# Optimization experiments

Measured on AMD Instinct MI355X. Metric: run time of the kernel, lower is better.

Reference implementation:

```python
import jax, jax.numpy as jnp
import numpy as np

T, H, F, E, K = 1024, 1024, 2048, 8, 2  # tokens, hidden, ffn_inter, experts, top_k


def setup_inputs() -> dict:
    key = jax.random.key(0)
    ks = jax.random.split(key, 7)
    return {
        "hidden_states": jax.random.normal(ks[0], (T, H), dtype=jnp.float32),
        "token_selected_experts": jax.random.randint(ks[1], (T, K), 0, E, dtype=jnp.int32),
        "token_final_scales": jax.random.uniform(ks[2], (T, K), dtype=jnp.float32),
        "w1": jax.random.normal(ks[3], (E, 2 * F, H), dtype=jnp.float32) * 0.02,  # gated fc1: [gate; linear]
        "b1": jax.random.normal(ks[4], (E, 2 * F), dtype=jnp.float32) * 0.02,
        "w2": jax.random.normal(ks[5], (E, H, F), dtype=jnp.float32) * 0.02,
        "b2": jax.random.normal(ks[6], (E, H), dtype=jnp.float32) * 0.02,
    }


def reference(hidden_states, token_selected_experts, token_final_scales, w1, b1, w2, b2):
    # Grouped GEMM fc1 over all experts: [T, E, 2F]
    h1 = jnp.einsum('th,efh->tef', hidden_states, w1) + b1[None]
    ffn = w2.shape[2]
    gate, lin = h1[..., :ffn], h1[..., ffn:]
    act = jax.nn.silu(gate) * lin                      # swiglu gated activation, [T, E, F]
    y_all = jnp.einsum('tef,ehf->teh', act, w2) + b2[None]  # fc2, [T, E, H]
    # Gather the top-k selected experts per token and combine with final scales
    sel = token_selected_experts.astype(jnp.int32)     # [T, K]
    y_sel = jnp.take_along_axis(y_all, sel[:, :, None], axis=1)  # [T, K, H]
    out = jnp.sum(y_sel * token_final_scales[:, :, None], axis=1)  # [T, H]
    return out
```

## Files before the change

kernel.cpp:

```cpp
#include <hip/hip_runtime.h>
#include <hip/hip_bf16.h>
#include <cstdint>
#include <cstddef>

#define TDIM 1024
#define HDIM 1024
#define FDIM 2048
#define NEXP 8
#define NENT 2048

typedef __bf16 bf16_t;
typedef __bf16 bf16x4 __attribute__((ext_vector_type(4)));
typedef __bf16 bf16x8 __attribute__((ext_vector_type(8)));
typedef float  f32x4  __attribute__((ext_vector_type(4)));

#define H_ELEMS  ((size_t)TDIM*HDIM)
#define W1_ELEMS ((size_t)NEXP*2*FDIM*HDIM)
#define W2_ELEMS ((size_t)NEXP*HDIM*FDIM)

#define WB_OFFSETS 0
#define WB_ETOK    64
#define WB_ESCALE  (WB_ETOK + NENT*4)
#define WB_ACT     16512
#define WB_H       (WB_ACT + (size_t)NENT*FDIM*2)
#define WB_W2BF    (WB_H + H_ELEMS*2)
#define WB_W1BF    (WB_W2BF + W2_ELEMS*2)
#define WB_NEED    (WB_W1BF + W1_ELEMS*2)

__device__ __forceinline__ void gload16(const void* g, void* l) {
  __builtin_amdgcn_global_load_lds((const __attribute__((address_space(1))) void*)g,
                                   (__attribute__((address_space(3))) void*)l, 16, 0, 0);
}

__device__ __forceinline__ bf16x8 cvt8(const float4 a, const float4 b) {
  bf16x8 o;
  o[0]=(bf16_t)a.x; o[1]=(bf16_t)a.y; o[2]=(bf16_t)a.z; o[3]=(bf16_t)a.w;
  o[4]=(bf16_t)b.x; o[5]=(bf16_t)b.y; o[6]=(bf16_t)b.z; o[7]=(bf16_t)b.w;
  return o;
}

__device__ __forceinline__ int segswz(int seg, int row) {
  return seg ^ (row & 3) ^ ((row >> 2) & 3);
}

__global__ void route_all(const int* __restrict__ sel, const float* __restrict__ scal,
                          int* __restrict__ offsets, int* __restrict__ etok,
                          float* __restrict__ escale) {
  __shared__ int cnt[NEXP], cnt2[NEXP], offs[NEXP+1];
  const int t = threadIdx.x;
  if (t < NEXP) { cnt[t] = 0; cnt2[t] = 0; }
  __syncthreads();
  int e8[8];
  #pragma unroll
  for (int q = 0; q < 8; q++) {
    int i = t*8 + q;
    e8[q] = sel[i];
    atomicAdd(&cnt[e8[q]], 1);
  }
  __syncthreads();
  if (t == 0) {
    int s = 0;
    for (int e = 0; e < NEXP; e++) { offs[e] = s; offsets[e] = s; s += cnt[e]; }
    offs[NEXP] = s; offsets[NEXP] = s;
  }
  __syncthreads();
  #pragma unroll
  for (int q = 0; q < 8; q++) {
    int i = t*8 + q;
    int e = e8[q];
    int pos = offs[e] + atomicAdd(&cnt2[e], 1);
    etok[pos]   = i >> 1;
    escale[pos] = scal[i];
  }
}

__global__ void convert_h(const float* __restrict__ h, bf16_t* __restrict__ hbf) {
  size_t idx = ((size_t)blockIdx.x*256 + threadIdx.x) * 8;
  float4 v0 = ((const float4*)(h + idx))[0];
  float4 v1 = ((const float4*)(h + idx))[1];
  *(bf16x8*)(hbf + idx) = cvt8(v0, v1);
}


__global__ __launch_bounds__(256, 3) void gemm1_v10(
    const bf16_t* __restrict__ hbf, const bf16_t* __restrict__ w1bf,
    const float* __restrict__ b1, const int* __restrict__ offsets,
    const int* __restrict__ etok, bf16_t* __restrict__ act)
{
  const int e   = blockIdx.y;
  const int off = offsets[e];
  const int nt  = offsets[e+1] - off;
  const int m0  = blockIdx.z * 128;
  if (m0 >= nt) return;
  const int n0  = blockIdx.x * 64;

  __shared__ __align__(16) bf16_t As[2][128*32];
  __shared__ __align__(16) bf16_t Bg[2][64*32];
  __shared__ __align__(16) bf16_t Bl[2][64*32];

  const int tid  = threadIdx.x;
  const int w    = tid >> 6, lane = tid & 63;
  const int quad = lane >> 4, lr = lane & 15;
  const int wm   = w >> 1,  wn = w & 1;

  const bf16_t* asrc0; const bf16_t* asrc1;
  int arow0, arow1;
  {
    const int r0 = 0*64 + w*16 + (lane >> 2);
    const int r1 = 1*64 + w*16 + (lane >> 2);
    const int s0 = segswz(lane & 3, r0);
    const int s1 = segswz(lane & 3, r1);
    int e0 = m0 + r0; if (e0 > nt-1) e0 = nt-1;
    int e1 = m0 + r1; if (e1 > nt-1) e1 = nt-1;
    asrc0 = hbf + (size_t)etok[off + e0]*HDIM + s0*8;
    asrc1 = hbf + (size_t)etok[off + e1]*HDIM + s1*8;
    arow0 = (0*64 + w*16)*32;
    arow1 = (1*64 + w*16)*32;
  }

  const bf16_t* gsrc; const bf16_t* lsrc;
  int bdst;
  {
    const int brow = w*16 + (lane >> 2);
    const int bseg = segswz(lane & 3, brow);
    gsrc = w1bf + ((size_t)e*2*FDIM + (size_t)(n0 + brow))*HDIM + bseg*8;
    lsrc = gsrc + (size_t)FDIM*HDIM;
    bdst = (w*16)*32;
  }

  int aoff[4], boff[2];
  #pragma unroll
  for (int i = 0; i < 4; i++) {
    const int r = wm*64 + i*16 + lr;
    aoff[i] = r*32 + (segswz(quad, r) << 3);
  }
  #pragma unroll
  for (int j = 0; j < 2; j++) {
    const int r = wn*32 + j*16 + lr;
    boff[j] = r*32 + (segswz(quad, r) << 3);
  }

  f32x4 accg[4][2] = {}, accl[4][2] = {};

#define G1_STAGE(K0, NXT)                                                     \
  { gload16(asrc0 + (K0), &As[NXT][arow0]);                                   \
    gload16(asrc1 + (K0), &As[NXT][arow1]);                                   \
    gload16(gsrc  + (K0), &Bg[NXT][bdst]);                                    \
    gload16(lsrc  + (K0), &Bl[NXT][bdst]); }

#define G1_MFMA(CUR)                                                          \
  { bf16x8 af[4], gf[2], lf[2];                                               \
    _Pragma("unroll")                                                         \
    for (int i = 0; i < 4; i++) af[i] = *(const bf16x8*)&As[CUR][aoff[i]];    \
    _Pragma("unroll")                                                         \
    for (int j = 0; j < 2; j++) {                                             \
      gf[j] = *(const bf16x8*)&Bg[CUR][boff[j]];                              \
      lf[j] = *(const bf16x8*)&Bl[CUR][boff[j]];                              \
    }                                                                         \
    _Pragma("unroll")                                                         \
    for (int i = 0; i < 4; i++)                                               \
      _Pragma("unroll")                                                       \
      for (int j = 0; j < 2; j++) {                                           \
        accg[i][j] = __builtin_amdgcn_mfma_f32_16x16x32_bf16(af[i], gf[j], accg[i][j], 0, 0, 0); \
        accl[i][j] = __builtin_amdgcn_mfma_f32_16x16x32_bf16(af[i], lf[j], accl[i][j], 0, 0, 0); \
      } }

#define G1_STEP(CUR)                                                          \
  { G1_STAGE(k0 + 32, (CUR)^1);                                               \
    __builtin_amdgcn_sched_barrier(0);                                        \
    G1_MFMA(CUR);                                                             \
    asm volatile("s_waitcnt vmcnt(0)" ::: "memory");                          \
    __builtin_amdgcn_sched_barrier(0);                                        \
    __builtin_amdgcn_s_barrier();                                             \
    __builtin_amdgcn_sched_barrier(0);                                        \
    k0 += 32; }

  G1_STAGE(0, 0);
  asm volatile("s_waitcnt vmcnt(0)" ::: "memory");
  __builtin_amdgcn_sched_barrier(0);
  __builtin_amdgcn_s_barrier();
  __builtin_amdgcn_sched_barrier(0);

  int k0 = 0;
  while (k0 < 960) {
    G1_STEP(0);
    G1_STEP(1);
  }
  G1_STEP(0);
  G1_MFMA(1);

#undef G1_STEP
#undef G1_MFMA
#undef G1_STAGE

  #pragma unroll
  for (int j = 0; j < 2; j++) {
    const int f = n0 + wn*32 + j*16 + lr;
    const float bg_ = b1[e*2*FDIM + f];
    const float bl_ = b1[e*2*FDIM + FDIM + f];
    #pragma unroll
    for (int i = 0; i < 4; i++) {
      #pragma unroll
      for (int r = 0; r < 4; r++) {
        const int m = wm*64 + i*16 + quad*4 + r;
        if (m0 + m < nt) {
          const float g = accg[i][j][r] + bg_;
          const float l = accl[i][j][r] + bl_;
          const float s = g / (1.f + __expf(-g)) * l;
          act[(size_t)(off + m0 + m)*FDIM + f] = (bf16_t)s;
        }
      }
    }
  }
}

__global__ __launch_bounds__(256, 3) void gemm2_v10(
    const bf16_t* __restrict__ act, const bf16_t* __restrict__ w2bf,
    const float* __restrict__ b2, const int* __restrict__ offsets,
    const int* __restrict__ etok, const float* __restrict__ escale,
    float* __restrict__ out)
{
  const int e   = blockIdx.y;
  const int off = offsets[e];
  const int nt  = offsets[e+1] - off;
  const int m0  = blockIdx.z * 128;
  if (m0 >= nt) return;
  const int n0  = (blockIdx.x >> 2) * 128;
  const int kc  = blockIdx.x & 3;
  const int kbeg = kc * (FDIM/4);

  __shared__ __align__(16) bf16_t As[2][128*32];
  __shared__ __align__(16) bf16_t Bs[2][128*32];

  const int tid  = threadIdx.x;
  const int w    = tid >> 6, lane = tid & 63;
  const int quad = lane >> 4, lr = lane & 15;
  const int wm   = w >> 1,  wn = w & 1;

  const bf16_t* asrc0; const bf16_t* asrc1;
  int arow0, arow1;
  {
    const int r0 = 0*64 + w*16 + (lane >> 2);
    const int r1 = 1*64 + w*16 + (lane >> 2);
    const int s0 = segswz(lane & 3, r0);
    const int s1 = segswz(lane & 3, r1);
    int e0 = m0 + r0; if (e0 > nt-1) e0 = nt-1;
    int e1 = m0 + r1; if (e1 > nt-1) e1 = nt-1;
    asrc0 = act + (size_t)(off + e0)*FDIM + kbeg + s0*8;
    asrc1 = act + (size_t)(off + e1)*FDIM + kbeg + s1*8;
    arow0 = (0*64 + w*16)*32;
    arow1 = (1*64 + w*16)*32;
  }

  const bf16_t* bsrc0; const bf16_t* bsrc1;
  int bdst0, bdst1;
  {
    const int r0 = w*32 + (lane >> 2);
    const int r1 = w*32 + 16 + (lane >> 2);
    const int s0 = segswz(lane & 3, r0);
    const int s1 = segswz(lane & 3, r1);
    bsrc0 = w2bf + ((size_t)e*HDIM + (size_t)(n0 + r0))*FDIM + kbeg + s0*8;
    bsrc1 = w2bf + ((size_t)e*HDIM + (size_t)(n0 + r1))*FDIM + kbeg + s1*8;
    bdst0 = (w*32)*32;
    bdst1 = (w*32 + 16)*32;
  }

  int aoff[4], boff[4];
  #pragma unroll
  for (int i = 0; i < 4; i++) {
    const int r = wm*64 + i*16 + lr;
    aoff[i] = r*32 + (segswz(quad, r) << 3);
  }
  #pragma unroll
  for (int j = 0; j < 4; j++) {
    const int r = wn*64 + j*16 + lr;
    boff[j] = r*32 + (segswz(quad, r) << 3);
  }

  f32x4 acc[4][4] = {};

#define G2_STAGE(K0, NXT)                                                     \
  { gload16(asrc0 + (K0), &As[NXT][arow0]);                                   \
    gload16(asrc1 + (K0), &As[NXT][arow1]);                                   \
    gload16(bsrc0 + (K0), &Bs[NXT][bdst0]);                                   \
    gload16(bsrc1 + (K0), &Bs[NXT][bdst1]); }

#define G2_MFMA(CUR)                                                          \
  { bf16x8 af[4], bfr[4];                                                     \
    _Pragma("unroll")                                                         \
    for (int i = 0; i < 4; i++) af[i] = *(const bf16x8*)&As[CUR][aoff[i]];    \
    _Pragma("unroll")                                                         \
    for (int j = 0; j < 4; j++) bfr[j] = *(const bf16x8*)&Bs[CUR][boff[j]];   \
    _Pragma("unroll")                                                         \
    for (int i = 0; i < 4; i++)                                               \
      _Pragma("unroll")                                                       \
      for (int j = 0; j < 4; j++)                                             \
        acc[i][j] = __builtin_amdgcn_mfma_f32_16x16x32_bf16(af[i], bfr[j], acc[i][j], 0, 0, 0); }

#define G2_STEP(CUR)                                                          \
  { G2_STAGE(k0 + 32, (CUR)^1);                                               \
    __builtin_amdgcn_sched_barrier(0);                                        \
    G2_MFMA(CUR);                                                             \
    asm volatile("s_waitcnt vmcnt(0)" ::: "memory");                          \
    __builtin_amdgcn_sched_barrier(0);                                        \
    __builtin_amdgcn_s_barrier();                                             \
    __builtin_amdgcn_sched_barrier(0);                                        \
    k0 += 32; }

  G2_STAGE(0, 0);
  asm volatile("s_waitcnt vmcnt(0)" ::: "memory");
  __builtin_amdgcn_sched_barrier(0);
  __builtin_amdgcn_s_barrier();
  __builtin_amdgcn_sched_barrier(0);

  int k0 = 0;
  while (k0 < 448) {
    G2_STEP(0);
    G2_STEP(1);
  }
  G2_STEP(0);
  G2_MFMA(1);

#undef G2_STEP
#undef G2_MFMA
#undef G2_STAGE

  #pragma unroll
  for (int i = 0; i < 4; i++) {
    #pragma unroll
    for (int r = 0; r < 4; r++) {
      const int m = wm*64 + i*16 + quad*4 + r;
      if (m0 + m < nt) {
        const int slot = off + m0 + m;
        const int t    = etok[slot];
        const float s  = escale[slot];
        #pragma unroll
        for (int j = 0; j < 4; j++) {
          const int n = n0 + wn*64 + j*16 + lr;
          float v = acc[i][j][r];
          if (kc == 0) v += b2[e*HDIM + n];
          atomicAdd(&out[(size_t)t*HDIM + n], s * v);
        }
      }
    }
  }
}

__global__ __launch_bounds__(256, 3) void gemm1_v8(
    const bf16_t* __restrict__ hbf, const float* __restrict__ w1,
    const float* __restrict__ b1, const int* __restrict__ offsets,
    const int* __restrict__ etok, bf16_t* __restrict__ act)
{
  const int e   = blockIdx.y;
  const int off = offsets[e];
  const int nt  = offsets[e+1] - off;
  const int m0  = blockIdx.z * 128;
  if (m0 >= nt) return;
  const int n0  = blockIdx.x * 64;

  __shared__ __align__(16) bf16_t As[2][128*32];
  __shared__ __align__(16) bf16_t Bg[2][64*32];
  __shared__ __align__(16) bf16_t Bl[2][64*32];

  const int tid  = threadIdx.x;
  const int w    = tid >> 6, lane = tid & 63;
  const int quad = lane >> 4, lr = lane & 15;
  const int wm   = w >> 1,  wn = w & 1;

  const bf16_t* asrc0; const bf16_t* asrc1;
  int arow0, arow1;
  {
    const int r0 = 0*64 + w*16 + (lane >> 2);
    const int r1 = 1*64 + w*16 + (lane >> 2);
    const int s0 = segswz(lane & 3, r0);
    const int s1 = segswz(lane & 3, r1);
    int e0 = m0 + r0; if (e0 > nt-1) e0 = nt-1;
    int e1 = m0 + r1; if (e1 > nt-1) e1 = nt-1;
    asrc0 = hbf + (size_t)etok[off + e0]*HDIM + s0*8;
    asrc1 = hbf + (size_t)etok[off + e1]*HDIM + s1*8;
    arow0 = (0*64 + w*16)*32;
    arow1 = (1*64 + w*16)*32;
  }

  const int br = tid >> 2, bs = tid & 3;
  const float* gsrc = w1 + ((size_t)e*2*FDIM + (size_t)(n0 + br))*HDIM + bs*8;
  const float* lsrc = gsrc + (size_t)FDIM*HDIM;
  const int bofs = br*32 + (segswz(bs, br) << 3);

  int aoff[4], boff[2];
  #pragma unroll
  for (int i = 0; i < 4; i++) {
    const int r = wm*64 + i*16 + lr;
    aoff[i] = r*32 + (segswz(quad, r) << 3);
  }
  #pragma unroll
  for (int j = 0; j < 2; j++) {
    const int r = wn*32 + j*16 + lr;
    boff[j] = r*32 + (segswz(quad, r) << 3);
  }

  f32x4 accg[4][2] = {}, accl[4][2] = {};
  float4 g4[2][2], l4[2][2];

#define F1_LOADB(SET, K0)                                                     \
  { const float4* p_ = (const float4*)(gsrc + (K0));                          \
    g4[SET][0]=p_[0]; g4[SET][1]=p_[1];                                       \
    const float4* q_ = (const float4*)(lsrc + (K0));                          \
    l4[SET][0]=q_[0]; l4[SET][1]=q_[1]; }
#define F1_WRITEB(NXT, SET)                                                   \
  { *(bf16x8*)&Bg[NXT][bofs] = cvt8(g4[SET][0], g4[SET][1]);                  \
    *(bf16x8*)&Bl[NXT][bofs] = cvt8(l4[SET][0], l4[SET][1]); }
#define F1_MFMA(CUR)                                                          \
  { bf16x8 af[4], gf[2], lf[2];                                               \
    _Pragma("unroll")                                                         \
    for (int i = 0; i < 4; i++) af[i] = *(const bf16x8*)&As[CUR][aoff[i]];    \
    _Pragma("unroll")                                                         \
    for (int j = 0; j < 2; j++) {                                             \
      gf[j] = *(const bf16x8*)&Bg[CUR][boff[j]];                              \
      lf[j] = *(const bf16x8*)&Bl[CUR][boff[j]];                              \
    }                                                                         \
    _Pragma("unroll")                                                         \
    for (int i = 0; i < 4; i++)                                               \
      _Pragma("unroll")                                                       \
      for (int j = 0; j < 2; j++) {                                           \
        accg[i][j] = __builtin_amdgcn_mfma_f32_16x16x32_bf16(af[i], gf[j], accg[i][j], 0, 0, 0); \
        accl[i][j] = __builtin_amdgcn_mfma_f32_16x16x32_bf16(af[i], lf[j], accl[i][j], 0, 0, 0); \
      } }

  F1_LOADB(0, 0);
  __builtin_amdgcn_sched_barrier(0);
  gload16(asrc0 + 0, &As[0][arow0]);
  gload16(asrc1 + 0, &As[0][arow1]);
  __builtin_amdgcn_sched_barrier(0);
  F1_WRITEB(0, 0);
  F1_LOADB(0, 32);
  F1_LOADB(1, 64);
  asm volatile("s_waitcnt vmcnt(8) lgkmcnt(0)" ::: "memory");
  __builtin_amdgcn_sched_barrier(0);
  __builtin_amdgcn_s_barrier();
  __builtin_amdgcn_sched_barrier(0);

#define F1_STEP(CUR, SET)                                                     \
  { F1_WRITEB((CUR)^1, SET);                                                  \
    __builtin_amdgcn_sched_barrier(0);                                        \
    gload16(asrc0 + k0 + 32, &As[(CUR)^1][arow0]);                            \
    gload16(asrc1 + k0 + 32, &As[(CUR)^1][arow1]);                            \
    __builtin_amdgcn_sched_barrier(0);                                        \
    F1_LOADB(SET, k0 + 96);                                                   \
    __builtin_amdgcn_sched_barrier(0);                                        \
    F1_MFMA(CUR);                                                             \
    asm volatile("s_waitcnt vmcnt(4) lgkmcnt(0)" ::: "memory");               \
    __builtin_amdgcn_sched_barrier(0);                                        \
    __builtin_amdgcn_s_barrier();                                             \
    __builtin_amdgcn_sched_barrier(0);                                        \
    k0 += 32; }

  int k0 = 0;
  while (k0 < 896) { F1_STEP(0, 0); F1_STEP(1, 1); }
  F1_STEP(0, 0);
  F1_WRITEB(0, 1);
  __builtin_amdgcn_sched_barrier(0);
  gload16(asrc0 + 960, &As[0][arow0]);
  gload16(asrc1 + 960, &As[0][arow1]);
  __builtin_amdgcn_sched_barrier(0);
  F1_MFMA(1);
  asm volatile("s_waitcnt vmcnt(0) lgkmcnt(0)" ::: "memory");
  __builtin_amdgcn_sched_barrier(0);
  __builtin_amdgcn_s_barrier();
  __builtin_amdgcn_sched_barrier(0);
  F1_WRITEB(1, 0);
  __builtin_amdgcn_sched_barrier(0);
  gload16(asrc0 + 992, &As[1][arow0]);
  gload16(asrc1 + 992, &As[1][arow1]);
  __builtin_amdgcn_sched_barrier(0);
  F1_MFMA(0);
  asm volatile("s_waitcnt vmcnt(0) lgkmcnt(0)" ::: "memory");
  __builtin_amdgcn_sched_barrier(0);
  __builtin_amdgcn_s_barrier();
  __builtin_amdgcn_sched_barrier(0);
  F1_MFMA(1);

#undef F1_STEP
#undef F1_MFMA
#undef F1_WRITEB
#undef F1_LOADB

  #pragma unroll
  for (int j = 0; j < 2; j++) {
    const int f = n0 + wn*32 + j*16 + lr;
    const float bg_ = b1[e*2*FDIM + f];
    const float bl_ = b1[e*2*FDIM + FDIM + f];
    #pragma unroll
    for (int i = 0; i < 4; i++) {
      #pragma unroll
      for (int r = 0; r < 4; r++) {
        const int m = wm*64 + i*16 + quad*4 + r;
        if (m0 + m < nt) {
          const float g = accg[i][j][r] + bg_;
          const float l = accl[i][j][r] + bl_;
          const float s = g / (1.f + __expf(-g)) * l;
          act[(size_t)(off + m0 + m)*FDIM + f] = (bf16_t)s;
        }
      }
    }
  }
}

__global__ __launch_bounds__(256, 3) void gemm2_v8(
    const bf16_t* __restrict__ act, const float* __restrict__ w2,
    const float* __restrict__ b2, const int* __restrict__ offsets,
    const int* __restrict__ etok, const float* __restrict__ escale,
    float* __restrict__ out)
{
  const int e   = blockIdx.y;
  const int off = offsets[e];
  const int nt  = offsets[e+1] - off;
  const int m0  = blockIdx.z * 128;
  if (m0 >= nt) return;
  const int n0  = (blockIdx.x >> 2) * 128;
  const int kc  = blockIdx.x & 3;
  const int kbeg = kc * (FDIM/4);

  __shared__ __align__(16) bf16_t As[2][128*32];
  __shared__ __align__(16) bf16_t Bs[2][128*32];

  const int tid  = threadIdx.x;
  const int w    = tid >> 6, lane = tid & 63;
  const int quad = lane >> 4, lr = lane & 15;
  const int wm   = w >> 1,  wn = w & 1;

  const bf16_t* asrc0; const bf16_t* asrc1;
  int arow0, arow1;
  {
    const int r0 = 0*64 + w*16 + (lane >> 2);
    const int r1 = 1*64 + w*16 + (lane >> 2);
    const int s0 = segswz(lane & 3, r0);
    const int s1 = segswz(lane & 3, r1);
    int e0 = m0 + r0; if (e0 > nt-1) e0 = nt-1;
    int e1 = m0 + r1; if (e1 > nt-1) e1 = nt-1;
    asrc0 = act + (size_t)(off + e0)*FDIM + kbeg + s0*8;
    asrc1 = act + (size_t)(off + e1)*FDIM + kbeg + s1*8;
    arow0 = (0*64 + w*16)*32;
    arow1 = (1*64 + w*16)*32;
  }

  const int br = tid >> 1, bc = tid & 1;
  const float* bsrc = w2 + ((size_t)e*HDIM + (size_t)(n0 + br))*FDIM + kbeg + bc*16;
  const int bofs0 = br*32 + (segswz(2*bc,   br) << 3);
  const int bofs1 = br*32 + (segswz(2*bc+1, br) << 3);

  int aoff[4], boff[4];
  #pragma unroll
  for (int i = 0; i < 4; i++) {
    const int r = wm*64 + i*16 + lr;
    aoff[i] = r*32 + (segswz(quad, r) << 3);
  }
  #pragma unroll
  for (int j = 0; j < 4; j++) {
    const int r = wn*64 + j*16 + lr;
    boff[j] = r*32 + (segswz(quad, r) << 3);
  }

  f32x4 acc[4][4] = {};
  float4 b4[2][4];

#define F2_LOADB(SET, K0)                                                     \
  { const float4* p_ = (const float4*)(bsrc + (K0));                          \
    b4[SET][0]=p_[0]; b4[SET][1]=p_[1]; b4[SET][2]=p_[2]; b4[SET][3]=p_[3]; }
#define F2_WRITEB(NXT, SET)                                                   \
  { *(bf16x8*)&Bs[NXT][bofs0] = cvt8(b4[SET][0], b4[SET][1]);                 \
    *(bf16x8*)&Bs[NXT][bofs1] = cvt8(b4[SET][2], b4[SET][3]); }
#define F2_MFMA(CUR)                                                          \
  { bf16x8 af[4], bfr[4];                                                     \
    _Pragma("unroll")                                                         \
    for (int i = 0; i < 4; i++) af[i] = *(const bf16x8*)&As[CUR][aoff[i]];    \
    _Pragma("unroll")                                                         \
    for (int j = 0; j < 4; j++) bfr[j] = *(const bf16x8*)&Bs[CUR][boff[j]];   \
    _Pragma("unroll")                                                         \
    for (int i = 0; i < 4; i++)                                               \
      _Pragma("unroll")                                                       \
      for (int j = 0; j < 4; j++)                                             \
        acc[i][j] = __builtin_amdgcn_mfma_f32_16x16x32_bf16(af[i], bfr[j], acc[i][j], 0, 0, 0); }

  F2_LOADB(0, 0);
  __builtin_amdgcn_sched_barrier(0);
  gload16(asrc0 + 0, &As[0][arow0]);
  gload16(asrc1 + 0, &As[0][arow1]);
  __builtin_amdgcn_sched_barrier(0);
  F2_WRITEB(0, 0);
  F2_LOADB(0, 32);
  F2_LOADB(1, 64);
  asm volatile("s_waitcnt vmcnt(8) lgkmcnt(0)" ::: "memory");
  __builtin_amdgcn_sched_barrier(0);
  __builtin_amdgcn_s_barrier();
  __builtin_amdgcn_sched_barrier(0);

#define F2_STEP(CUR, SET)                                                     \
  { F2_WRITEB((CUR)^1, SET);                                                  \
    __builtin_amdgcn_sched_barrier(0);                                        \
    gload16(asrc0 + k0 + 32, &As[(CUR)^1][arow0]);                            \
    gload16(asrc1 + k0 + 32, &As[(CUR)^1][arow1]);                            \
    __builtin_amdgcn_sched_barrier(0);                                        \
    F2_LOADB(SET, k0 + 96);                                                   \
    __builtin_amdgcn_sched_barrier(0);                                        \
    F2_MFMA(CUR);                                                             \
    asm volatile("s_waitcnt vmcnt(4) lgkmcnt(0)" ::: "memory");               \
    __builtin_amdgcn_sched_barrier(0);                                        \
    __builtin_amdgcn_s_barrier();                                             \
    __builtin_amdgcn_sched_barrier(0);                                        \
    k0 += 32; }

  int k0 = 0;
  while (k0 < 384) { F2_STEP(0, 0); F2_STEP(1, 1); }
  F2_STEP(0, 0);
  F2_WRITEB(0, 1);
  __builtin_amdgcn_sched_barrier(0);
  gload16(asrc0 + 448, &As[0][arow0]);
  gload16(asrc1 + 448, &As[0][arow1]);
  __builtin_amdgcn_sched_barrier(0);
  F2_MFMA(1);
  asm volatile("s_waitcnt vmcnt(0) lgkmcnt(0)" ::: "memory");
  __builtin_amdgcn_sched_barrier(0);
  __builtin_amdgcn_s_barrier();
  __builtin_amdgcn_sched_barrier(0);
  F2_WRITEB(1, 0);
  __builtin_amdgcn_sched_barrier(0);
  gload16(asrc0 + 480, &As[1][arow0]);
  gload16(asrc1 + 480, &As[1][arow1]);
  __builtin_amdgcn_sched_barrier(0);
  F2_MFMA(0);
  asm volatile("s_waitcnt vmcnt(0) lgkmcnt(0)" ::: "memory");
  __builtin_amdgcn_sched_barrier(0);
  __builtin_amdgcn_s_barrier();
  __builtin_amdgcn_sched_barrier(0);
  F2_MFMA(1);

#undef F2_STEP
#undef F2_MFMA
#undef F2_WRITEB
#undef F2_LOADB

  #pragma unroll
  for (int i = 0; i < 4; i++) {
    #pragma unroll
    for (int r = 0; r < 4; r++) {
      const int m = wm*64 + i*16 + quad*4 + r;
      if (m0 + m < nt) {
        const int slot = off + m0 + m;
        const int t    = etok[slot];
        const float s  = escale[slot];
        #pragma unroll
        for (int j = 0; j < 4; j++) {
          const int n = n0 + wn*64 + j*16 + lr;
          float v = acc[i][j][r];
          if (kc == 0) v += b2[e*HDIM + n];
          atomicAdd(&out[(size_t)t*HDIM + n], s * v);
        }
      }
    }
  }
}

extern "C" void kernel_launch(void* const* d_in, const int* in_sizes, int n_in,
                              void* d_out, int out_size, void* d_ws, size_t ws_size,
                              hipStream_t stream) {
  const float* hidden = (const float*)d_in[0];
  const int*   sel    = (const int*)d_in[1];
  const float* scal   = (const float*)d_in[2];
  const float* w1     = (const float*)d_in[3];
  const float* b1     = (const float*)d_in[4];
  const float* w2     = (const float*)d_in[5];
  const float* b2     = (const float*)d_in[6];
  float* out = (float*)d_out;

  char* ws = (char*)d_ws;
  int*    offsets = (int*)(ws + WB_OFFSETS);
  int*    etok    = (int*)(ws + WB_ETOK);
  float*  escale  = (float*)(ws + WB_ESCALE);
  bf16_t* act     = (bf16_t*)(ws + WB_ACT);
  bf16_t* hbf     = (bf16_t*)(ws + WB_H);
  bf16_t* w2bf    = (bf16_t*)(ws + WB_W2BF);
  bf16_t* w1bf    = (bf16_t*)(ws + WB_W1BF);

  hipMemsetAsync(d_out, 0, (size_t)out_size * sizeof(float), stream);

  route_all<<<1, 256, 0, stream>>>(sel, scal, offsets, etok, escale);
  convert_h<<<(int)(H_ELEMS/8/256), 256, 0, stream>>>(hidden, hbf);

  if (ws_size >= WB_NEED) {
    convert_h<<<(int)(W2_ELEMS/8/256), 256, 0, stream>>>(w2, w2bf);
    convert_h<<<(int)(W1_ELEMS/8/256), 256, 0, stream>>>(w1, w1bf);
    gemm1_v10<<<dim3(FDIM/64, NEXP, NENT/128), 256, 0, stream>>>(hbf, w1bf, b1, offsets, etok, act);
    gemm2_v10<<<dim3((HDIM/128)*4, NEXP, NENT/128), 256, 0, stream>>>(act, w2bf, b2, offsets, etok, escale, out);
  } else {
    gemm1_v8<<<dim3(FDIM/64, NEXP, NENT/128), 256, 0, stream>>>(hbf, w1, b1, offsets, etok, act);
    gemm2_v8<<<dim3((HDIM/128)*4, NEXP, NENT/128), 256, 0, stream>>>(act, w2, b2, offsets, etok, escale, out);
  }
}
```

Measured before the change: 358.3 us.

## Triple-buffer LDS staging in both expert GEMMs with prefetch distance two

Both grouped GEMM kernels move from double to triple shared-memory buffers and issue global-to-LDS loads two K-steps ahead. The per-step wait relaxes from vmcnt(0) to vmcnt(4), so one stage's loads can stay in flight while the MFMAs run. The goal is to hide more global-load latency behind compute. The cost is more LDS per block, which could limit occupancy at 3 blocks per CU, plus more complex prologue and epilogue scheduling.

```diff
diff --git a/kernel.cpp b/kernel.cpp
--- a/kernel.cpp
+++ b/kernel.cpp
@@ -82,7 +82,7 @@
 }
 
 
-__global__ __launch_bounds__(256, 3) void gemm1_v10(
+__global__ __launch_bounds__(256, 3) void gemm1_v11(
     const bf16_t* __restrict__ hbf, const bf16_t* __restrict__ w1bf,
     const float* __restrict__ b1, const int* __restrict__ offsets,
     const int* __restrict__ etok, bf16_t* __restrict__ act)
@@ -94,9 +94,9 @@
   if (m0 >= nt) return;
   const int n0  = blockIdx.x * 64;
 
-  __shared__ __align__(16) bf16_t As[2][128*32];
-  __shared__ __align__(16) bf16_t Bg[2][64*32];
-  __shared__ __align__(16) bf16_t Bl[2][64*32];
+  __shared__ __align__(16) bf16_t As[3][128*32];
+  __shared__ __align__(16) bf16_t Bg[3][64*32];
+  __shared__ __align__(16) bf16_t Bl[3][64*32];
 
   const int tid  = threadIdx.x;
   const int w    = tid >> 6, lane = tid & 63;
@@ -165,28 +165,34 @@
         accl[i][j] = __builtin_amdgcn_mfma_f32_16x16x32_bf16(af[i], lf[j], accl[i][j], 0, 0, 0); \
       } }
 
-#define G1_STEP(CUR)                                                          \
-  { G1_STAGE(k0 + 32, (CUR)^1);                                               \
+#define G1_STEP(CUR, NXT)                                                     \
+  { G1_STAGE(k0 + 64, NXT);                                                   \
     __builtin_amdgcn_sched_barrier(0);                                        \
     G1_MFMA(CUR);                                                             \
-    asm volatile("s_waitcnt vmcnt(0)" ::: "memory");                          \
+    asm volatile("s_waitcnt vmcnt(4)" ::: "memory");                          \
     __builtin_amdgcn_sched_barrier(0);                                        \
     __builtin_amdgcn_s_barrier();                                             \
     __builtin_amdgcn_sched_barrier(0);                                        \
     k0 += 32; }
 
   G1_STAGE(0, 0);
-  asm volatile("s_waitcnt vmcnt(0)" ::: "memory");
+  G1_STAGE(32, 1);
+  asm volatile("s_waitcnt vmcnt(4)" ::: "memory");
   __builtin_amdgcn_sched_barrier(0);
   __builtin_amdgcn_s_barrier();
   __builtin_amdgcn_sched_barrier(0);
 
   int k0 = 0;
   while (k0 < 960) {
-    G1_STEP(0);
-    G1_STEP(1);
-  }
-  G1_STEP(0);
+    G1_STEP(0, 2);
+    G1_STEP(1, 0);
+    G1_STEP(2, 1);
+  }
+  G1_MFMA(0);
+  asm volatile("s_waitcnt vmcnt(0)" ::: "memory");
+  __builtin_amdgcn_sched_barrier(0);
+  __builtin_amdgcn_s_barrier();
+  __builtin_amdgcn_sched_barrier(0);
   G1_MFMA(1);
 
 #undef G1_STEP
@@ -214,7 +220,7 @@
   }
 }
 
-__global__ __launch_bounds__(256, 3) void gemm2_v10(
+__global__ __launch_bounds__(256, 3) void gemm2_v11(
     const bf16_t* __restrict__ act, const bf16_t* __restrict__ w2bf,
     const float* __restrict__ b2, const int* __restrict__ offsets,
     const int* __restrict__ etok, const float* __restrict__ escale,
@@ -229,8 +235,8 @@
   const int kc  = blockIdx.x & 3;
   const int kbeg = kc * (FDIM/4);
 
-  __shared__ __align__(16) bf16_t As[2][128*32];
-  __shared__ __align__(16) bf16_t Bs[2][128*32];
+  __shared__ __align__(16) bf16_t As[3][128*32];
+  __shared__ __align__(16) bf16_t Bs[3][128*32];
 
   const int tid  = threadIdx.x;
   const int w    = tid >> 6, lane = tid & 63;
@@ -297,29 +303,37 @@
       for (int j = 0; j < 4; j++)                                             \
         acc[i][j] = __builtin_amdgcn_mfma_f32_16x16x32_bf16(af[i], bfr[j], acc[i][j], 0, 0, 0); }
 
-#define G2_STEP(CUR)                                                          \
-  { G2_STAGE(k0 + 32, (CUR)^1);                                               \
+#define G2_STEP(CUR, NXT)                                                     \
+  { G2_STAGE(k0 + 64, NXT);                                                   \
     __builtin_amdgcn_sched_barrier(0);                                        \
     G2_MFMA(CUR);                                                             \
-    asm volatile("s_waitcnt vmcnt(0)" ::: "memory");                          \
+    asm volatile("s_waitcnt vmcnt(4)" ::: "memory");                          \
     __builtin_amdgcn_sched_barrier(0);                                        \
     __builtin_amdgcn_s_barrier();                                             \
     __builtin_amdgcn_sched_barrier(0);                                        \
     k0 += 32; }
 
   G2_STAGE(0, 0);
+  G2_STAGE(32, 1);
+  asm volatile("s_waitcnt vmcnt(4)" ::: "memory");
+  __builtin_amdgcn_sched_barrier(0);
+  __builtin_amdgcn_s_barrier();
+  __builtin_amdgcn_sched_barrier(0);
+
+  int k0 = 0;
+  while (k0 < 384) {
+    G2_STEP(0, 2);
+    G2_STEP(1, 0);
+    G2_STEP(2, 1);
+  }
+  G2_STEP(0, 2);
+  G2_STEP(1, 0);
+  G2_MFMA(2);
   asm volatile("s_waitcnt vmcnt(0)" ::: "memory");
   __builtin_amdgcn_sched_barrier(0);
   __builtin_amdgcn_s_barrier();
   __builtin_amdgcn_sched_barrier(0);
-
-  int k0 = 0;
-  while (k0 < 448) {
-    G2_STEP(0);
-    G2_STEP(1);
-  }
-  G2_STEP(0);
-  G2_MFMA(1);
+  G2_MFMA(0);
 
 #undef G2_STEP
 #undef G2_MFMA
@@ -690,8 +704,8 @@
   if (ws_size >= WB_NEED) {
     convert_h<<<(int)(W2_ELEMS/8/256), 256, 0, stream>>>(w2, w2bf);
     convert_h<<<(int)(W1_ELEMS/8/256), 256, 0, stream>>>(w1, w1bf);
-    gemm1_v10<<<dim3(FDIM/64, NEXP, NENT/128), 256, 0, stream>>>(hbf, w1bf, b1, offsets, etok, act);
-    gemm2_v10<<<dim3((HDIM/128)*4, NEXP, NENT/128), 256, 0, stream>>>(act, w2bf, b2, offsets, etok, escale, out);
+    gemm1_v11<<<dim3(FDIM/64, NEXP, NENT/128), 256, 0, stream>>>(hbf, w1bf, b1, offsets, etok, act);
+    gemm2_v11<<<dim3((HDIM/128)*4, NEXP, NENT/128), 256, 0, stream>>>(act, w2bf, b2, offsets, etok, escale, out);
   } else {
     gemm1_v8<<<dim3(FDIM/64, NEXP, NENT/128), 256, 0, stream>>>(hbf, w1, b1, offsets, etok, act);
     gemm2_v8<<<dim3((HDIM/128)*4, NEXP, NENT/128), 256, 0, stream>>>(act, w2, b2, offsets, etok, escale, out);
```

New measurement: 356.9 us. No clear change (-0.4%).
